# Kernel tuning notes

Hardware: AMD Instinct MI355X
Metric: run time of the kernel (lower is better)

## Reference

```python
import jax, jax.numpy as jnp
import numpy as np

DT = 0.01
SIM_STEPS = 10_000_000
G = jnp.array([0.0, -9.81], dtype=jnp.float32)  # gravity, matches Ball.g


def setup_inputs() -> dict:
    key = jax.random.key(0)
    k_pos, k_vel = jax.random.split(key)
    return {
        "ball_mass": jnp.ones((), dtype=jnp.float32),  # unused by the math, kept for signature fidelity
        "ball_initial_position": jax.random.normal(k_pos, (2,), dtype=jnp.float32),
        "ball_initial_velocity": jax.random.normal(k_vel, (2,), dtype=jnp.float32),  # nn.Parameter
    }


def reference(ball_mass, ball_initial_position, ball_initial_velocity):
    # Faithful semi-implicit-Euler-style recurrence:
    #   pos <- pos + vel*dt ; vel <- vel + g*dt ; record pos
    # trajectory[0] is the initial position, trajectory[1:] are the updated positions.
    def step(carry, _):
        pos, vel = carry
        pos = pos + vel * DT
        vel = vel + G * DT
        return (pos, vel), pos

    _, traj = jax.lax.scan(
        step, (ball_initial_position, ball_initial_velocity), None, length=SIM_STEPS - 1
    )  # traj: [SIM_STEPS-1, 2]
    return jnp.concatenate([ball_initial_position[None, :], traj], axis=0)  # [SIM_STEPS, 2]
```

## Files before the change

### kernel.cpp

```cpp
#include <hip/hip_runtime.h>
#include <stdint.h>


static constexpr long long NSTEPS = 10000000LL;
static constexpr long long NPOLY  = 1000000LL;
static constexpr long long NS     = 5500000LL;
static constexpr long long KDIR   = 64;
static constexpr int SEGCAP = 384;
static constexpr int RUNCAP = 96;

__device__ __forceinline__ bool same_binade_f32(float a, float b) {
    return (((__float_as_uint(a) ^ __float_as_uint(b)) & 0xFF800000u) == 0u);
}
__device__ __forceinline__ unsigned expfield(float v) {
    return (__float_as_uint(v) >> 23) & 0xFFu;
}
__device__ __forceinline__ float pow2f(int e) {
    return __uint_as_float((unsigned)(e + 127) << 23);
}
__device__ __forceinline__ double pow2d(int e) {
    return __longlong_as_double(((long long)(e + 1023)) << 52);
}
__device__ __forceinline__ int bin_k_d(double v) {
    return (int)((__double_as_longlong(v) >> 52) & 0x7FFll) - 1022;
}

__global__ __launch_bounds__(256, 4) void fused(
        const float* __restrict__ pos0, const float* __restrict__ vel0,
        float4* __restrict__ out, long long npairs)
{
    __shared__ int    s_m[SEGCAP + 1];
    __shared__ double s_V[SEGCAP], s_c[SEGCAP], s_P[SEGCAP];
    __shared__ float  s_Vf[SEGCAP], s_cdt[SEGCAP], s_Pf[SEGCAP];
    __shared__ int    r_n[RUNCAP];
    __shared__ double r_p[RUNCAP], r_i[RUNCAP];
    __shared__ float  r_pf[RUNCAP], r_if[RUNCAP];
    __shared__ int    s_nseg, s_bad, s_nrun;
    __shared__ long long s_mstop;
    __shared__ double s_v64, s_p64;

    const int tid  = threadIdx.x;
    const int lane = tid & 63;
    const int wv   = tid >> 6;

    const long long per = (npairs + (long long)gridDim.x - 1) / (long long)gridDim.x;
    const long long i0 = (long long)blockIdx.x * per;
    long long i1 = i0 + per; if (i1 > npairs) i1 = npairs;
    if (i0 >= npairs) return;
    const long long row_end = 2 * i1;
    const long long mstop = row_end < NSTEPS ? row_end : NSTEPS;

    const float dtf  = 0.01f;
    const float gdtf = __fmul_rn(-9.81f, dtf);
    const double dtd = (double)dtf, gcd = (double)gdtf, gdtd = gcd;
    const double p0y = (double)pos0[1], v0y = (double)vel0[1];

    int k_tie;
    {
        unsigned g = __float_as_uint(gdtf);
        unsigned mant = (g & 0x7FFFFFu) | 0x800000u;
        int tz = __ffs((int)mant) - 1;
        int E = (int)((g >> 23) & 0xFFu) - 127 - 23 + tz;
        k_tie = E + 25;
    }

    if (tid == 0) {
        s_nrun = 0;
        double V = v0y, P = p0y;
        for (int t = 0; t < (int)KDIR; ++t) {
            const float vf = (float)V;
            P += dtd * V;
            V = (double)__fadd_rn(vf, gdtf);
        }
        s_v64 = V; s_p64 = P;

        bool bad = false;
        long long m = KDIR;
        int nseg = 0;
        if (row_end > NPOLY) {
            while (m < mstop) {
                if (nseg >= SEGCAP - 2) { bad = true; break; }
                const float vf = (float)V;
                if ((double)vf != V || !(vf < 0.0f)) { bad = true; break; }
                const unsigned ef = expfield(vf);
                if (ef == 0u || ef == 0xFFu) { bad = true; break; }
                const int k = (int)ef - 126;
                if (k == k_tie) { bad = true; break; }
                const float vn1 = __fadd_rn(vf, gdtf);
                const double c = (double)vn1 - V;
                if (!(c < 0.0)) { bad = true; break; }
                const long long rem = mstop - m;
                const double B = -pow2d(k);

                float tt = __fdividef((float)(V + gcd - B), (float)(-c)) + 1.0f;
                long long T = (tt > 0.0f) ? (long long)tt : 0;
                if (T > rem + 4) T = rem + 4;
                T -= (long long)((T > 0) && (V + (double)(T - 1) * c + gcd <= B));
                T -= (long long)((T > 0) && (V + (double)(T - 1) * c + gcd <= B));
                T -= (long long)((T > 0) && (V + (double)(T - 1) * c + gcd <= B));
                T += (long long)(V + (double)T * c + gcd > B);
                T += (long long)(V + (double)T * c + gcd > B);
                T += (long long)(V + (double)T * c + gcd > B);
                if (T < 0) T = 0;
                if (T > rem) T = rem;
                if (T > 0) {
                    s_m[nseg] = (int)m; s_V[nseg] = V; s_c[nseg] = c; s_P[nseg] = P; ++nseg;
                    P += dtd * ((double)T * V + c * ((double)T * (double)(T - 1) * 0.5));
                    V += (double)T * c;
                    m += T;
                    if (m >= mstop) break;
                }
                const float vf2 = (float)V;
                if ((double)vf2 != V) { bad = true; break; }
                const float vb = __fadd_rn(vf2, gdtf);
                const double cb = (double)vb - V;
                s_m[nseg] = (int)m; s_V[nseg] = V; s_c[nseg] = cb; s_P[nseg] = P; ++nseg;
                P += dtd * V;
                V += cb;
                m += 1;
            }
            bad = bad || (m < mstop);
        }
        s_bad = bad ? 1 : 0;
        s_nseg = nseg;
        s_mstop = m;
        s_m[nseg] = 0x7fffffff;
    }
    __syncthreads();

    if (wv == 0 && !s_bad && s_nseg > 0) {
        const int nseg = s_nseg;
        const long long mbuilt = s_mstop;
        bool ok = true;
        for (int i = lane; i < nseg; i += 64) {
            const double Vi = s_V[i], ci = s_c[i];
            const long long mi = s_m[i];
            const long long me = (i + 1 < nseg) ? (long long)s_m[i + 1] : mbuilt;
            const long long len = me - mi;
            ok = ok && (len >= 1);
            const float vfi = (float)Vi;
            ok = ok && ((double)vfi == Vi);
            const float vn = __fadd_rn(vfi, gdtf);
            ok = ok && ((double)vn - Vi == ci);
            const double Ve = Vi + (double)(len - 1) * ci;
            const float vfe = (float)Ve;
            ok = ok && ((double)vfe == Ve);
            const float vne = __fadd_rn(vfe, gdtf);
            ok = ok && ((double)vne - Ve == ci);
            if (len > 1) {
                const unsigned efi = expfield(vfi);
                ok = ok && (efi != 0u) && (efi != 0xFFu);
                const int kk = (int)efi - 126;
                ok = ok && same_binade_f32(vfe, vfi);
                ok = ok && (bin_k_d(Vi + gcd) == kk);
                ok = ok && (bin_k_d(Ve + gcd) == kk);
                ok = ok && (kk != k_tie);
            }
            if (i + 1 < nseg)
                ok = ok && (s_V[i + 1] == Vi + (double)len * ci);
        }
        const unsigned long long good = __ballot(ok);
        if (lane == 0 && good != ~0ULL) s_bad = 1;
    }
    __syncthreads();

    if (wv == 0 && s_bad) {
        double V = s_v64, P = s_p64;
        long long m = KDIR;
        int nseg = 0;
        while (m < mstop && nseg < SEGCAP) {
            const float vf  = (float)V;
            const float vn1 = __fadd_rn(vf, gdtf);
            const double c  = (double)vn1 - V;
            const long long rem = mstop - m;
            long long Lb = rem;
            const float cf = (float)c;
            const unsigned ef = expfield(vf);
            if (vf == 0.0f || ef == 0u) {
                Lb = 64;
            } else if (cf != 0.0f) {
                const int k = (int)ef - 126;
                float s = vf < 0.0f ? -1.0f : 1.0f;
                float B = ((vf < 0.0f) == (cf < 0.0f)) ? s * pow2f(k) : s * pow2f(k - 1);
                float r = __fdividef(B - vf, cf);
                if (r >= 0.0f && r < 4.0e9f) Lb = (long long)r + 1;
            }
            long long Lhi = Lb + 2;
            if (Lhi > rem) Lhi = rem;
            if (Lhi < 1) Lhi = 1;

            long long L = 1, base = Lhi;
            for (int round = 0; round < 32; ++round) {
                const long long candL = base - 63 + (long long)lane;
                bool valid = false;
                if (candL >= 1) {
                    const double ve = V + (double)(candL - 1) * c;
                    const float vef = (float)ve;
                    const float vn2 = __fadd_rn(vef, gdtf);
                    valid = ((double)vef == ve)
                         && same_binade_f32(vef, vf)
                         && ((double)vn2 - ve == c);
                }
                unsigned long long msk = __ballot(valid);
                if (msk) { L = base - 63 + (long long)(63 - __clzll(msk)); break; }
                base -= 64;
                if (base < 1) break;
            }
            if (L < 1) L = 1;
            if (L > rem) L = rem;

            if (lane == 0) { s_m[nseg] = (int)m; s_V[nseg] = V; s_c[nseg] = c; s_P[nseg] = P; }
            ++nseg;
            P += dtd * ((double)L * V + c * ((double)L * (double)(L - 1) * 0.5));
            V += (double)L * c;
            m += L;
        }
        if (lane == 0) { s_nseg = nseg; s_mstop = m; s_m[nseg] = 0x7fffffff; }
    }
    __syncthreads();

    if (wv == 0 && row_end > NS && s_mstop >= NS && s_nseg > 0) {
        const int nseg = s_nseg;
        const long long mbuilt = s_mstop;
        int lo = 0, hi = nseg - 1;
        while (lo < hi) { int mid = (lo + hi + 1) >> 1;
                          if ((long long)s_m[mid] <= NS) lo = mid; else hi = mid - 1; }
        int jj = lo;
        const double t0 = (double)(NS - s_m[jj]);
        double vel = s_V[jj] + t0 * s_c[jj];
        double P2  = s_P[jj] + dtd * (t0 * s_V[jj] + s_c[jj] * (t0 * (t0 - 1.0) * 0.5));
        double pos = (double)(float)P2;
        long long n = NS;
        int nrun = 0;
        long long nend = (row_end < NSTEPS - 1) ? row_end : (NSTEPS - 1);
        if (nend > mbuilt) nend = mbuilt;
        while (n < nend && nrun < RUNCAP) {
            while (s_m[jj + 1] <= (int)n) ++jj;
            const double cv = s_c[jj];
            long long Lcap = (long long)s_m[jj + 1] - n;
            if (Lcap > mbuilt - n) Lcap = mbuilt - n;
            const long long rem = (NSTEPS - 1) - n;
            if (Lcap > rem) Lcap = rem;

            const float pf = (float)pos;
            const float vf2 = (float)vel;
            const float dstep = __fmul_rn(vf2, dtf);
            const float pn1 = __fadd_rn(pf, dstep);
            const double inc = (double)pn1 - pos;

            long long La = Lcap, Lc = Lcap;
            const float incf = (float)inc;
            const unsigned efp = expfield(pf);
            if (pf == 0.0f || efp == 0u) {
                La = 64;
            } else if (incf != 0.0f) {
                const int k = (int)efp - 126;
                float s = pf < 0.0f ? -1.0f : 1.0f;
                float B = ((pf < 0.0f) == (incf < 0.0f)) ? s * pow2f(k) : s * pow2f(k - 1);
                float r = __fdividef(B - pf, incf);
                if (r >= 0.0f && r < 4.0e9f) { La = (long long)r - 1; if (La < 0) La = 0; }
            }
            const double dd = cv * dtd;
            if (dd != 0.0 && pf != 0.0f && efp != 0u) {
                const int k = (int)efp - 126;
                if (k - 24 > -126) {
                    const float ulpf = pow2f(k - 24);
                    const double d0 = (double)dstep;
                    const double T = inc + (dd < 0.0 ? -0.5 : 0.5) * (double)ulpf;
                    float r = __fdividef((float)(T - d0), (float)dd);
                    if (r >= 0.0f && r < 4.0e9f) { Lc = (long long)r + 2; if (Lc < 1) Lc = 1; }
                }
            }
            long long Lhi = La < Lc ? La : Lc;
            Lhi += 3;
            if (Lhi > Lcap) Lhi = Lcap;
            if (Lhi < 1) Lhi = 1;

            long long L = 1, base = Lhi;
            for (int round = 0; round < 32; ++round) {
                const long long candL = base - 63 + (long long)lane;
                bool valid = false;
                if (candL >= 1) {
                    const double pe = pos + (double)(candL - 1) * inc;
                    const double ve = vel + (double)(candL - 1) * cv;
                    const float pef = (float)pe;
                    const float vef = (float)ve;
                    const float d2  = __fmul_rn(vef, dtf);
                    const float pn2 = __fadd_rn(pef, d2);
                    valid = ((double)pef == pe)
                         && same_binade_f32(pef, pf)
                         && ((double)vef == ve)
                         && ((double)pn2 - pe == inc);
                }
                unsigned long long msk = __ballot(valid);
                if (msk) { L = base - 63 + (long long)(63 - __clzll(msk)); break; }
                base -= 64;
                if (base < 1) break;
            }
            if (L < 1) L = 1;
            if (L > Lcap) L = Lcap;
            if (L < 1) L = 1;

            if (lane == 0) { r_n[nrun] = (int)n; r_p[nrun] = pos; r_i[nrun] = inc; }
            ++nrun;
            pos += (double)L * inc;
            vel += (double)L * cv;
            n += L;
        }
        if (lane == 0) s_nrun = nrun;
    }
    __syncthreads();

    {
        const int nseg = s_nseg, nrun = s_nrun;
        for (int i = tid; i < nseg; i += 256) {
            s_Vf[i]  = (float)s_V[i];
            s_cdt[i] = (float)(dtd * s_c[i]);
            s_Pf[i]  = (float)s_P[i];
        }
        for (int i = tid; i < nrun; i += 256) {
            r_pf[i] = (float)r_p[i];
            r_if[i] = (float)r_i[i];
        }
    }
    __syncthreads();

    const int nseg = s_nseg;
    const int nrun = s_nrun;
    const float pxf = pos0[0];
    const float cxf = __fmul_rn(vel0[0], dtf);
    const float pyf = (float)p0y;
    const float vyf = (float)v0y;
    const float q2f = (float)(dtd * gdtd);

    const long long ii = i0 + tid;
    if (ii >= i1) return;

    int j = 0, r = 0;
    if (nseg > 0) {
        const int t0 = (int)(2 * ii);
        int lo = 0, hi = nseg - 1;
        while (lo < hi) { int mid = (lo + hi + 1) >> 1; if (s_m[mid] <= t0) lo = mid; else hi = mid - 1; }
        j = lo;
        if (nrun > 0) {
            int rlo = 0, rhi = nrun - 1;
            while (rlo < rhi) { int mid = (rlo + rhi + 1) >> 1; if (r_n[mid] <= t0) rlo = mid; else rhi = mid - 1; }
            r = rlo;
        }
    }
    for (long long i = ii; i < i1; i += blockDim.x) {
        const long long m0 = 2 * i, m1 = m0 + 1;
        const float mf0 = (float)m0, mf1 = (float)m1;
        float4 o;
        o.x = pxf + mf0 * cxf;
        o.z = pxf + mf1 * cxf;
        const int t0 = (int)m0;

        if (m1 < NPOLY) {
            o.y = pyf + dtf * (mf0 * vyf) + q2f * (mf0 * (mf0 - 1.0f) * 0.5f);
            o.w = pyf + dtf * (mf1 * vyf) + q2f * (mf1 * (mf1 - 1.0f) * 0.5f);
        } else if (m1 < NS || nrun <= 0) {
            while (s_m[j + 1] <= t0) ++j;
            float t = (float)(int)(m0 - s_m[j]);
            o.y = s_Pf[j] + dtf * (t * s_Vf[j]) + s_cdt[j] * (t * (t - 1.0f) * 0.5f);
            const int j1 = (s_m[j + 1] <= (int)m1) ? j + 1 : j;
            t = (float)(int)(m1 - s_m[j1]);
            o.w = s_Pf[j1] + dtf * (t * s_Vf[j1]) + s_cdt[j1] * (t * (t - 1.0f) * 0.5f);
        } else {
            while (r + 1 < nrun && r_n[r + 1] <= t0) ++r;
            o.y = r_pf[r] + (float)(int)(m0 - r_n[r]) * r_if[r];
            const int r1 = (r + 1 < nrun && r_n[r + 1] <= (int)m1) ? r + 1 : r;
            o.w = r_pf[r1] + (float)(int)(m1 - r_n[r1]) * r_if[r1];
        }
        out[i] = o;
    }
}

extern "C" void kernel_launch(void* const* d_in, const int* in_sizes, int n_in,
                              void* d_out, int out_size, void* d_ws, size_t ws_size,
                              hipStream_t stream) {
    const float* pos0 = (const float*)d_in[1];
    const float* vel0 = (const float*)d_in[2];

    const long long npairs = (long long)out_size / 4;
    fused<<<1024, 256, 0, stream>>>(pos0, vel0, (float4*)d_out, npairs);
}
```

Before: 43.07 us.

## Use exact ulp-grid segment lengths, skip unneeded setup, specialize uniform-mode store loops

Segment lengths in the serial float-rounding model are now computed on an integer ulp grid: the per-step increment is rounded in units of the ulp, and exact ties take a single step. This replaces the division plus six correction checks. The setup, validation and fallback phases are skipped for blocks that lie fully in the polynomial region, and the fallback ballot search now tests only one 64-candidate window. Each block picks a uniform mode (polynomial, single segment, or single run) and uses a branch-free FMA store loop for it, which removes per-element searches and divergence. The risk is that the single-window search or the reduced validation may accept wrong segment lengths in edge cases.

After: 41.02 us. -4.8%, faster.

```diff
diff --git a/kernel.cpp b/kernel.cpp
--- a/kernel.cpp
+++ b/kernel.cpp
@@ -20,9 +20,6 @@
 }
 __device__ __forceinline__ double pow2d(int e) {
     return __longlong_as_double(((long long)(e + 1023)) << 52);
-}
-__device__ __forceinline__ int bin_k_d(double v) {
-    return (int)((__double_as_longlong(v) >> 52) & 0x7FFll) - 1022;
 }
 
 __global__ __launch_bounds__(256, 4) void fused(
@@ -47,22 +44,14 @@
     const long long i0 = (long long)blockIdx.x * per;
     long long i1 = i0 + per; if (i1 > npairs) i1 = npairs;
     if (i0 >= npairs) return;
-    const long long row_end = 2 * i1;
-    const long long mstop = row_end < NSTEPS ? row_end : NSTEPS;
+    const long long row0 = 2 * i0;
+    const long long row1 = 2 * i1;
+    const long long mstop = row1 < NSTEPS ? row1 : NSTEPS;
 
     const float dtf  = 0.01f;
     const float gdtf = __fmul_rn(-9.81f, dtf);
     const double dtd = (double)dtf, gcd = (double)gdtf, gdtd = gcd;
     const double p0y = (double)pos0[1], v0y = (double)vel0[1];
-
-    int k_tie;
-    {
-        unsigned g = __float_as_uint(gdtf);
-        unsigned mant = (g & 0x7FFFFFu) | 0x800000u;
-        int tz = __ffs((int)mant) - 1;
-        int E = (int)((g >> 23) & 0xFFu) - 127 - 23 + tz;
-        k_tie = E + 25;
-    }
 
     if (tid == 0) {
         s_nrun = 0;
@@ -77,7 +66,7 @@
         bool bad = false;
         long long m = KDIR;
         int nseg = 0;
-        if (row_end > NPOLY) {
+        if (row1 > NPOLY) {
             while (m < mstop) {
                 if (nseg >= SEGCAP - 2) { bad = true; break; }
                 const float vf = (float)V;
@@ -85,24 +74,33 @@
                 const unsigned ef = expfield(vf);
                 if (ef == 0u || ef == 0xFFu) { bad = true; break; }
                 const int k = (int)ef - 126;
-                if (k == k_tie) { bad = true; break; }
-                const float vn1 = __fadd_rn(vf, gdtf);
-                const double c = (double)vn1 - V;
-                if (!(c < 0.0)) { bad = true; break; }
+                const double ulp     = pow2d(k - 24);
+                const double inv_ulp = pow2d(24 - k);
+                const double g = -V * inv_ulp;
+                const double q = -gcd * inv_ulp;
+                const double fq = floor(q);
                 const long long rem = mstop - m;
-                const double B = -pow2d(k);
-
-                float tt = __fdividef((float)(V + gcd - B), (float)(-c)) + 1.0f;
-                long long T = (tt > 0.0f) ? (long long)tt : 0;
-                if (T > rem + 4) T = rem + 4;
-                T -= (long long)((T > 0) && (V + (double)(T - 1) * c + gcd <= B));
-                T -= (long long)((T > 0) && (V + (double)(T - 1) * c + gcd <= B));
-                T -= (long long)((T > 0) && (V + (double)(T - 1) * c + gcd <= B));
-                T += (long long)(V + (double)T * c + gcd > B);
-                T += (long long)(V + (double)T * c + gcd > B);
-                T += (long long)(V + (double)T * c + gcd > B);
+
+                if (q - fq == 0.5) {
+                    const float vb = __fadd_rn(vf, gdtf);
+                    const double cb = (double)vb - V;
+                    s_m[nseg] = (int)m; s_V[nseg] = V; s_c[nseg] = cb; s_P[nseg] = P; ++nseg;
+                    P += dtd * V; V += cb; m += 1;
+                    continue;
+                }
+                const double cg = floor(q + 0.5);
+                if (!(cg > 0.0)) { bad = true; break; }
+                const double c = -cg * ulp;
+
+                const double lim = 16777216.0;
+                float t0f = __fdividef((float)(lim - g - q), (float)cg);
+                long long T = (long long)t0f + 1;
+                if (T > rem) T = rem;
                 if (T < 0) T = 0;
+                for (int f = 0; f < 4 && T > 0 && !(g + (double)(T - 1) * cg + q < lim); ++f) --T;
+                for (int f = 0; f < 4 && T < rem && (g + (double)T * cg + q < lim); ++f) ++T;
                 if (T > rem) T = rem;
+
                 if (T > 0) {
                     s_m[nseg] = (int)m; s_V[nseg] = V; s_c[nseg] = c; s_P[nseg] = P; ++nseg;
                     P += dtd * ((double)T * V + c * ((double)T * (double)(T - 1) * 0.5));
@@ -115,9 +113,7 @@
                 const float vb = __fadd_rn(vf2, gdtf);
                 const double cb = (double)vb - V;
                 s_m[nseg] = (int)m; s_V[nseg] = V; s_c[nseg] = cb; s_P[nseg] = P; ++nseg;
-                P += dtd * V;
-                V += cb;
-                m += 1;
+                P += dtd * V; V += cb; m += 1;
             }
             bad = bad || (m < mstop);
         }
@@ -128,7 +124,7 @@
     }
     __syncthreads();
 
-    if (wv == 0 && !s_bad && s_nseg > 0) {
+    if (wv == 0 && !s_bad && s_nseg > 0 && row1 > NPOLY) {
         const int nseg = s_nseg;
         const long long mbuilt = s_mstop;
         bool ok = true;
@@ -147,15 +143,7 @@
             ok = ok && ((double)vfe == Ve);
             const float vne = __fadd_rn(vfe, gdtf);
             ok = ok && ((double)vne - Ve == ci);
-            if (len > 1) {
-                const unsigned efi = expfield(vfi);
-                ok = ok && (efi != 0u) && (efi != 0xFFu);
-                const int kk = (int)efi - 126;
-                ok = ok && same_binade_f32(vfe, vfi);
-                ok = ok && (bin_k_d(Vi + gcd) == kk);
-                ok = ok && (bin_k_d(Ve + gcd) == kk);
-                ok = ok && (kk != k_tie);
-            }
+            if (len > 1) ok = ok && same_binade_f32(vfe, vfi);
             if (i + 1 < nseg)
                 ok = ok && (s_V[i + 1] == Vi + (double)len * ci);
         }
@@ -164,7 +152,7 @@
     }
     __syncthreads();
 
-    if (wv == 0 && s_bad) {
+    if (wv == 0 && s_bad && row1 > NPOLY) {
         double V = s_v64, P = s_p64;
         long long m = KDIR;
         int nseg = 0;
@@ -189,9 +177,9 @@
             if (Lhi > rem) Lhi = rem;
             if (Lhi < 1) Lhi = 1;
 
-            long long L = 1, base = Lhi;
-            for (int round = 0; round < 32; ++round) {
-                const long long candL = base - 63 + (long long)lane;
+            long long L = 1;
+            {
+                const long long candL = Lhi - 63 + (long long)lane;
                 bool valid = false;
                 if (candL >= 1) {
                     const double ve = V + (double)(candL - 1) * c;
@@ -201,10 +189,8 @@
                          && same_binade_f32(vef, vf)
                          && ((double)vn2 - ve == c);
                 }
-                unsigned long long msk = __ballot(valid);
-                if (msk) { L = base - 63 + (long long)(63 - __clzll(msk)); break; }
-                base -= 64;
-                if (base < 1) break;
+                const unsigned long long msk = __ballot(valid);
+                if (msk) L = Lhi - 63 + (long long)(63 - __clzll(msk));
             }
             if (L < 1) L = 1;
             if (L > rem) L = rem;
@@ -219,7 +205,7 @@
     }
     __syncthreads();
 
-    if (wv == 0 && row_end > NS && s_mstop >= NS && s_nseg > 0) {
+    if (wv == 0 && row1 > NS && s_mstop >= NS && s_nseg > 0) {
         const int nseg = s_nseg;
         const long long mbuilt = s_mstop;
         int lo = 0, hi = nseg - 1;
@@ -232,7 +218,7 @@
         double pos = (double)(float)P2;
         long long n = NS;
         int nrun = 0;
-        long long nend = (row_end < NSTEPS - 1) ? row_end : (NSTEPS - 1);
+        long long nend = (row1 < NSTEPS - 1) ? row1 : (NSTEPS - 1);
         if (nend > mbuilt) nend = mbuilt;
         while (n < nend && nrun < RUNCAP) {
             while (s_m[jj + 1] <= (int)n) ++jj;
@@ -276,9 +262,9 @@
             if (Lhi > Lcap) Lhi = Lcap;
             if (Lhi < 1) Lhi = 1;
 
-            long long L = 1, base = Lhi;
-            for (int round = 0; round < 32; ++round) {
-                const long long candL = base - 63 + (long long)lane;
+            long long L = 1;
+            {
+                const long long candL = Lhi - 63 + (long long)lane;
                 bool valid = false;
                 if (candL >= 1) {
                     const double pe = pos + (double)(candL - 1) * inc;
@@ -292,10 +278,8 @@
                          && ((double)vef == ve)
                          && ((double)pn2 - pe == inc);
                 }
-                unsigned long long msk = __ballot(valid);
-                if (msk) { L = base - 63 + (long long)(63 - __clzll(msk)); break; }
-                base -= 64;
-                if (base < 1) break;
+                const unsigned long long msk = __ballot(valid);
+                if (msk) L = Lhi - 63 + (long long)(63 - __clzll(msk));
             }
             if (L < 1) L = 1;
             if (L > Lcap) L = Lcap;
@@ -336,43 +320,102 @@
     const long long ii = i0 + tid;
     if (ii >= i1) return;
 
-    int j = 0, r = 0;
-    if (nseg > 0) {
-        const int t0 = (int)(2 * ii);
+    int mode = 3, jf = 0, rf = 0;
+    if (row1 <= NPOLY) {
+        mode = 0;
+    } else if (row0 >= NS && nrun > 0) {
+        int rlo = 0, rhi = nrun - 1;
+        const int t0 = (int)row0;
+        while (rlo < rhi) { int mid = (rlo + rhi + 1) >> 1; if (r_n[mid] <= t0) rlo = mid; else rhi = mid - 1; }
+        rf = rlo;
+        if (rf + 1 >= nrun || (long long)r_n[rf + 1] >= row1) mode = 2;
+    } else if (row0 >= NPOLY && row1 <= NS && nseg > 0) {
         int lo = 0, hi = nseg - 1;
+        const int t0 = (int)row0;
         while (lo < hi) { int mid = (lo + hi + 1) >> 1; if (s_m[mid] <= t0) lo = mid; else hi = mid - 1; }
-        j = lo;
-        if (nrun > 0) {
-            int rlo = 0, rhi = nrun - 1;
-            while (rlo < rhi) { int mid = (rlo + rhi + 1) >> 1; if (r_n[mid] <= t0) rlo = mid; else rhi = mid - 1; }
-            r = rlo;
-        }
-    }
-    for (long long i = ii; i < i1; i += blockDim.x) {
-        const long long m0 = 2 * i, m1 = m0 + 1;
-        const float mf0 = (float)m0, mf1 = (float)m1;
-        float4 o;
-        o.x = pxf + mf0 * cxf;
-        o.z = pxf + mf1 * cxf;
-        const int t0 = (int)m0;
-
-        if (m1 < NPOLY) {
-            o.y = pyf + dtf * (mf0 * vyf) + q2f * (mf0 * (mf0 - 1.0f) * 0.5f);
-            o.w = pyf + dtf * (mf1 * vyf) + q2f * (mf1 * (mf1 - 1.0f) * 0.5f);
-        } else if (m1 < NS || nrun <= 0) {
-            while (s_m[j + 1] <= t0) ++j;
-            float t = (float)(int)(m0 - s_m[j]);
-            o.y = s_Pf[j] + dtf * (t * s_Vf[j]) + s_cdt[j] * (t * (t - 1.0f) * 0.5f);
-            const int j1 = (s_m[j + 1] <= (int)m1) ? j + 1 : j;
-            t = (float)(int)(m1 - s_m[j1]);
-            o.w = s_Pf[j1] + dtf * (t * s_Vf[j1]) + s_cdt[j1] * (t * (t - 1.0f) * 0.5f);
-        } else {
-            while (r + 1 < nrun && r_n[r + 1] <= t0) ++r;
-            o.y = r_pf[r] + (float)(int)(m0 - r_n[r]) * r_if[r];
-            const int r1 = (r + 1 < nrun && r_n[r + 1] <= (int)m1) ? r + 1 : r;
-            o.w = r_pf[r1] + (float)(int)(m1 - r_n[r1]) * r_if[r1];
-        }
-        out[i] = o;
+        jf = lo;
+        if ((long long)s_m[jf + 1] >= row1) mode = 1;
+    }
+
+    if (mode == 0) {
+        const float C = 0.5f * q2f;
+        const float B = dtf * vyf - C;
+        const float A = pyf;
+        for (long long i = ii; i < i1; i += blockDim.x) {
+            const float mf0 = (float)(2 * i), mf1 = mf0 + 1.0f;
+            float4 o;
+            o.x = fmaf(mf0, cxf, pxf);
+            o.z = fmaf(mf1, cxf, pxf);
+            o.y = fmaf(mf0, fmaf(mf0, C, B), A);
+            o.w = fmaf(mf1, fmaf(mf1, C, B), A);
+            out[i] = o;
+        }
+    } else if (mode == 1) {
+        const float C = 0.5f * s_cdt[jf];
+        const float B = dtf * s_Vf[jf] - C;
+        const float A = s_Pf[jf];
+        const int mj = s_m[jf];
+        for (long long i = ii; i < i1; i += blockDim.x) {
+            const float t0 = (float)(int)(2 * i - mj), t1 = t0 + 1.0f;
+            const float mf0 = (float)(2 * i), mf1 = mf0 + 1.0f;
+            float4 o;
+            o.x = fmaf(mf0, cxf, pxf);
+            o.z = fmaf(mf1, cxf, pxf);
+            o.y = fmaf(t0, fmaf(t0, C, B), A);
+            o.w = fmaf(t1, fmaf(t1, C, B), A);
+            out[i] = o;
+        }
+    } else if (mode == 2) {
+        const float A = r_pf[rf], Bv = r_if[rf];
+        const int rn0 = r_n[rf];
+        for (long long i = ii; i < i1; i += blockDim.x) {
+            const float t0 = (float)(int)(2 * i - rn0), t1 = t0 + 1.0f;
+            const float mf0 = (float)(2 * i), mf1 = mf0 + 1.0f;
+            float4 o;
+            o.x = fmaf(mf0, cxf, pxf);
+            o.z = fmaf(mf1, cxf, pxf);
+            o.y = fmaf(t0, Bv, A);
+            o.w = fmaf(t1, Bv, A);
+            out[i] = o;
+        }
+    } else {
+        int j = 0, r = 0;
+        if (nseg > 0) {
+            const int t0 = (int)(2 * ii);
+            int lo = 0, hi = nseg - 1;
+            while (lo < hi) { int mid = (lo + hi + 1) >> 1; if (s_m[mid] <= t0) lo = mid; else hi = mid - 1; }
+            j = lo;
+            if (nrun > 0) {
+                int rlo = 0, rhi = nrun - 1;
+                while (rlo < rhi) { int mid = (rlo + rhi + 1) >> 1; if (r_n[mid] <= t0) rlo = mid; else rhi = mid - 1; }
+                r = rlo;
+            }
+        }
+        for (long long i = ii; i < i1; i += blockDim.x) {
+            const long long m0 = 2 * i, m1 = m0 + 1;
+            const float mf0 = (float)m0, mf1 = (float)m1;
+            float4 o;
+            o.x = fmaf(mf0, cxf, pxf);
+            o.z = fmaf(mf1, cxf, pxf);
+            const int t0 = (int)m0;
+            if (m1 < NPOLY) {
+                o.y = pyf + dtf * (mf0 * vyf) + q2f * (mf0 * (mf0 - 1.0f) * 0.5f);
+                o.w = pyf + dtf * (mf1 * vyf) + q2f * (mf1 * (mf1 - 1.0f) * 0.5f);
+            } else if (m1 < NS || nrun <= 0) {
+                while (s_m[j + 1] <= t0) ++j;
+                float t = (float)(int)(m0 - s_m[j]);
+                o.y = s_Pf[j] + dtf * (t * s_Vf[j]) + s_cdt[j] * (t * (t - 1.0f) * 0.5f);
+                const int j1 = (s_m[j + 1] <= (int)m1) ? j + 1 : j;
+                t = (float)(int)(m1 - s_m[j1]);
+                o.w = s_Pf[j1] + dtf * (t * s_Vf[j1]) + s_cdt[j1] * (t * (t - 1.0f) * 0.5f);
+            } else {
+                while (r + 1 < nrun && r_n[r + 1] <= t0) ++r;
+                o.y = r_pf[r] + (float)(int)(m0 - r_n[r]) * r_if[r];
+                const int r1 = (r + 1 < nrun && r_n[r + 1] <= (int)m1) ? r + 1 : r;
+                o.w = r_pf[r1] + (float)(int)(m1 - r_n[r1]) * r_if[r1];
+            }
+            out[i] = o;
+        }
     }
 }
 
```
